# Performance work log

Hardware: AMD Instinct MI355X
Metric: run time of the kernel (lower is better)

Reference implementation:

```python
import jax, jax.numpy as jnp
import numpy as np

B, S, H, NH = 16, 2048, 256, 4
HD = H // NH  # head_size = 64
NEG = -(2.0 ** 32) + 1.0


def _heads(x):
    # [B,S,H] -> [NH,B,S,HD], matching torch.cat(torch.split(x, HD, dim=2), dim=0)
    b, s, _ = x.shape
    return jnp.transpose(x.reshape(b, s, NH, HD), (2, 0, 1, 3))


def setup_inputs() -> dict:
    key = jax.random.key(0)
    ks = jax.random.split(key, 9)
    d = {
        "queries": jax.random.normal(ks[0], (B, S, H), jnp.float32),
        "keys": jax.random.normal(ks[1], (B, S, H), jnp.float32),
        "neighbor_matrix": jax.random.normal(ks[2], (B, S, H), jnp.float32),
        "neighAt_matrix": jax.random.normal(ks[3], (B, S, H), jnp.float32),
        "abs_pos_K": jax.random.normal(ks[4], (B, S, H), jnp.float32),
        "abs_pos_V": jax.random.normal(ks[5], (B, S, H), jnp.float32),
        # True = masked; causal mask (mask strictly-upper triangle)
        "attn_mask": jnp.triu(jnp.ones((S, S), bool), k=1),
        "Qw": jax.random.normal(ks[6], (H, H), jnp.float32) * (1.0 / np.sqrt(H)),
        "Qb": jnp.zeros((H,), jnp.float32),
        "Kw": jax.random.normal(ks[7], (H, H), jnp.float32) * (1.0 / np.sqrt(H)),
        "Kb": jnp.zeros((H,), jnp.float32),
        "Vw": jax.random.normal(ks[8], (H, H), jnp.float32) * (1.0 / np.sqrt(H)),
        "Vb": jnp.zeros((H,), jnp.float32),
    }
    return d


def reference(queries, keys, neighbor_matrix, neighAt_matrix, abs_pos_K, abs_pos_V,
              attn_mask, Qw, Qb, Kw, Kb, Vw, Vb):
    Q = queries @ Qw.T + Qb
    K = keys @ Kw.T + Kb
    V = keys @ Vw.T + Vb

    Qh = _heads(Q)                 # [NH,B,S,HD]
    Kh = _heads(K)
    Vh = _heads(V)
    Nh = _heads(neighbor_matrix)
    Ah = _heads(neighAt_matrix)
    PKh = _heads(abs_pos_K)
    PVh = _heads(abs_pos_V)

    # sum of four QX^T terms == Q @ (K+N+A+PK)^T  (distributivity)
    Ksum = Kh + Nh + Ah + PKh
    scores = jnp.einsum("hbqd,hbkd->hbqk", Qh, Ksum) / jnp.sqrt(jnp.float32(HD))
    scores = jnp.where(attn_mask[None, None], jnp.float32(NEG), scores)
    attn = jax.nn.softmax(scores, axis=-1)

    Vsum = Vh + Nh + Ah + PVh
    out = jnp.einsum("hbqk,hbkd->hbqd", attn, Vsum)   # [NH,B,S,HD]
    # recombine heads along feature dim
    return jnp.transpose(out, (1, 2, 0, 3)).reshape(B, S, H)
```

## Files before the change

### kernel.cpp

```cpp
#include <hip/hip_runtime.h>
#include <math.h>

#define BB 16
#define SS 2048
#define HH 256
#define NHEAD 4
#define HDIM 64

typedef _Float16 f16;
typedef _Float16 f16x2 __attribute__((ext_vector_type(2)));
typedef _Float16 f16x4 __attribute__((ext_vector_type(4)));
typedef _Float16 f16x8 __attribute__((ext_vector_type(8)));
typedef float f32x4 __attribute__((ext_vector_type(4)));

#define MFMA16(a, b, c) __builtin_amdgcn_mfma_f32_16x16x32_f16((a), (b), (c), 0, 0, 0)

__device__ __forceinline__ void split8(const float* p, f16x8& h, f16x8& lo) {
    float4 v0 = *(const float4*)p;
    float4 v1 = *(const float4*)(p + 4);
    float vv[8] = {v0.x, v0.y, v0.z, v0.w, v1.x, v1.y, v1.z, v1.w};
#pragma unroll
    for (int j = 0; j < 8; j++) {
        f16 hv = (f16)vv[j];
        h[j] = hv;
        lo[j] = (f16)(vv[j] - (float)hv);
    }
}

__global__ __launch_bounds__(512) void proj_kernel(
    const float* __restrict__ queries, const float* __restrict__ keys,
    const float* __restrict__ neighbor, const float* __restrict__ neighAt,
    const float* __restrict__ posK, const float* __restrict__ posV,
    const float* __restrict__ Qw, const float* __restrict__ Qb,
    const float* __restrict__ Kw, const float* __restrict__ Kb,
    const float* __restrict__ Vw, const float* __restrict__ Vb,
    f16* __restrict__ Qh, f16* __restrict__ Ql,
    f16* __restrict__ Kh, f16* __restrict__ Kl,
    f16* __restrict__ VTh, f16* __restrict__ VTl)
{
    const int z  = blockIdx.y;
    const int m0 = blockIdx.x * 128;

    const float* X    = (z == 0) ? queries : keys;
    const float* W    = (z == 0) ? Qw : (z == 1 ? Kw : Vw);
    const float* bias = (z == 0) ? Qb : (z == 1 ? Kb : Vb);

    __shared__ __align__(16) char smraw[61440];
    f16*   Xh_s = (f16*)smraw;
    f16*   Xl_s = Xh_s + 128 * 40;
    f16*   Wh_s = Xl_s + 128 * 40;
    f16*   Wl_s = Wh_s + 256 * 40;
    float* Ls   = (float*)smraw;

    const int t  = threadIdx.x;
    const int w  = t >> 6, l = t & 63, c = l & 15, g = l >> 4;
    const int wm = w >> 2, wn = w & 3;

    f32x4 acc[4][4];
#pragma unroll
    for (int i = 0; i < 4; i++)
#pragma unroll
        for (int j = 0; j < 4; j++) acc[i][j] = (f32x4){0.f, 0.f, 0.f, 0.f};

    const int xrow = t >> 2, xseg = t & 3;
    const int wrow = t >> 1, whalf = t & 1;

    for (int ks = 0; ks < 8; ks++) {
        const int k0 = ks * 32;
        __syncthreads();
        {
            f16x8 h, lo;
            split8(&X[(size_t)(m0 + xrow) * HH + k0 + xseg * 8], h, lo);
            *(f16x8*)&Xh_s[xrow * 40 + xseg * 8] = h;
            *(f16x8*)&Xl_s[xrow * 40 + xseg * 8] = lo;
        }
#pragma unroll
        for (int s2 = 0; s2 < 2; s2++) {
            f16x8 h, lo;
            split8(&W[(size_t)wrow * HH + k0 + whalf * 16 + s2 * 8], h, lo);
            *(f16x8*)&Wh_s[wrow * 40 + whalf * 16 + s2 * 8] = h;
            *(f16x8*)&Wl_s[wrow * 40 + whalf * 16 + s2 * 8] = lo;
        }
        __syncthreads();

        f16x8 ah[4], al[4], bh[4], bl[4];
#pragma unroll
        for (int fm = 0; fm < 4; fm++) {
            const int ro = (wm * 64 + fm * 16 + c) * 40 + g * 8;
            ah[fm] = *(const f16x8*)&Xh_s[ro];
            al[fm] = *(const f16x8*)&Xl_s[ro];
        }
#pragma unroll
        for (int fn = 0; fn < 4; fn++) {
            const int ro = (wn * 64 + fn * 16 + c) * 40 + g * 8;
            bh[fn] = *(const f16x8*)&Wh_s[ro];
            bl[fn] = *(const f16x8*)&Wl_s[ro];
        }
#pragma unroll
        for (int fm = 0; fm < 4; fm++)
#pragma unroll
            for (int fn = 0; fn < 4; fn++) {
                acc[fm][fn] = MFMA16(ah[fm], bh[fn], acc[fm][fn]);
                acc[fm][fn] = MFMA16(al[fm], bh[fn], acc[fm][fn]);
                acc[fm][fn] = MFMA16(ah[fm], bl[fn], acc[fm][fn]);
            }
    }

    const int bI  = m0 >> 11;
    const int s0g = m0 & (SS - 1);

#pragma unroll 1
    for (int p = 0; p < 4; p++) {
        __syncthreads();
        if (wm == (p >> 1)) {
            const int fmb = (p & 1) * 2;
#pragma unroll
            for (int fi = 0; fi < 2; fi++)
#pragma unroll
                for (int fn = 0; fn < 4; fn++)
#pragma unroll
                    for (int r = 0; r < 4; r++)
                        Ls[(fi * 16 + 4 * g + r) * 260 + wn * 64 + fn * 16 + c] =
                            acc[fmb + fi][fn][r];
        }
        __syncthreads();

        if (z <= 1) {
            f16* Xph = (z == 0) ? Qh : Kh;
            f16* Xpl = (z == 0) ? Ql : Kl;
#pragma unroll
            for (int i = 0; i < 4; i++) {
                int idx = t + 512 * i;
                int r = idx >> 6, q = idx & 63;
                float4 v  = *(const float4*)&Ls[r * 260 + q * 4];
                float4 bv = *(const float4*)&bias[q * 4];
                v.x += bv.x; v.y += bv.y; v.z += bv.z; v.w += bv.w;
                size_t gg = (size_t)(m0 + 32 * p + r) * HH + q * 4;
                if (z == 1) {
                    float4 n1 = *(const float4*)&neighbor[gg];
                    float4 n2 = *(const float4*)&neighAt[gg];
                    float4 n3 = *(const float4*)&posK[gg];
                    v.x += n1.x + n2.x + n3.x;  v.y += n1.y + n2.y + n3.y;
                    v.z += n1.z + n2.z + n3.z;  v.w += n1.w + n2.w + n3.w;
                }
                f16x4 hv, lv;
                hv[0] = (f16)v.x; hv[1] = (f16)v.y; hv[2] = (f16)v.z; hv[3] = (f16)v.w;
                lv[0] = (f16)(v.x - (float)hv[0]);
                lv[1] = (f16)(v.y - (float)hv[1]);
                lv[2] = (f16)(v.z - (float)hv[2]);
                lv[3] = (f16)(v.w - (float)hv[3]);
                *(f16x4*)(Xph + gg) = hv;
                *(f16x4*)(Xpl + gg) = lv;
            }
        } else {
#pragma unroll
            for (int i = 0; i < 4; i++) {
                int idx = t + 512 * i;
                int r = idx >> 6, q = idx & 63;
                float4 v  = *(const float4*)&Ls[r * 260 + q * 4];
                float4 bv = *(const float4*)&bias[q * 4];
                size_t gg = (size_t)(m0 + 32 * p + r) * HH + q * 4;
                float4 n1 = *(const float4*)&neighbor[gg];
                float4 n2 = *(const float4*)&neighAt[gg];
                float4 n3 = *(const float4*)&posV[gg];
                v.x += bv.x + n1.x + n2.x + n3.x;
                v.y += bv.y + n1.y + n2.y + n3.y;
                v.z += bv.z + n1.z + n2.z + n3.z;
                v.w += bv.w + n1.w + n2.w + n3.w;
                *(float4*)&Ls[r * 260 + q * 4] = v;
            }
            __syncthreads();
            const int n = t >> 1, soff = (t & 1) * 16;
            f16x8 h0, h1, l0, l1;
#pragma unroll
            for (int j = 0; j < 16; j++) {
                float val = Ls[(soff + j) * 260 + n];
                f16 hv = (f16)val;
                f16 lv = (f16)(val - (float)hv);
                if (j < 8) { h0[j] = hv; l0[j] = lv; }
                else       { h1[j - 8] = hv; l1[j - 8] = lv; }
            }
            size_t ga = ((size_t)n * BB + bI) * SS + s0g + 32 * p + soff;
            *(f16x8*)&VTh[ga]     = h0;
            *(f16x8*)&VTh[ga + 8] = h1;
            *(f16x8*)&VTl[ga]     = l0;
            *(f16x8*)&VTl[ga + 8] = l1;
        }
    }
}

__global__ __launch_bounds__(512) void attn_kernel(
    const f16* __restrict__ Qhg, const f16* __restrict__ Qlg,
    const f16* __restrict__ Khg, const f16* __restrict__ Klg,
    const f16* __restrict__ Vhg, const f16* __restrict__ Vlg,
    float* __restrict__ outp)
{
    const int bid = blockIdx.x;
    const int qt  = 15 - (bid >> 6);
    const int rem = bid & 63;
    const int b   = rem >> 2;
    const int h   = rem & 3;
    const int q0  = qt * 128;

    __shared__ __align__(16) f16 smh[46080];
    f16* Qh_s = smh;
    f16* Ql_s = smh + 9216;
    f16* Kh_s = smh + 18432;
    f16* Kl_s = smh + 23040;
    f16* Vh_s = smh + 27648;
    f16* Vl_s = smh + 32256;
    f16* Ps   = smh + 36864;

    const int t = threadIdx.x;

    {
        const size_t base = ((size_t)(b * SS) + q0) * HH + h * 64;
#pragma unroll
        for (int p = 0; p < 2; p++) {
            int idx = t + 512 * p;
            int row = idx >> 3, ch = idx & 7;
            size_t g = base + (size_t)row * HH + ch * 8;
            *(uint4*)&Qh_s[row * 72 + ch * 8] = *(const uint4*)&Qhg[g];
            *(uint4*)&Ql_s[row * 72 + ch * 8] = *(const uint4*)&Qlg[g];
        }
    }
    __syncthreads();

    const int w = t >> 6, l = t & 63, c = l & 15, g = l >> 4;

    f16x8 aQh[2], aQl[2];
#pragma unroll
    for (int dk = 0; dk < 2; dk++) {
        aQh[dk] = *(const f16x8*)&Qh_s[(16 * w + c) * 72 + dk * 32 + g * 8];
        aQl[dk] = *(const f16x8*)&Ql_s[(16 * w + c) * 72 + dk * 32 + g * 8];
    }

    f32x4 o[4] = {{0.f,0.f,0.f,0.f},{0.f,0.f,0.f,0.f},{0.f,0.f,0.f,0.f},{0.f,0.f,0.f,0.f}};
    float m_i[4] = {-INFINITY, -INFINITY, -INFINITY, -INFINITY};
    float l_i[4] = {0.f, 0.f, 0.f, 0.f};

    const int nkv = 2 * qt + 2;
    for (int kt = 0; kt < nkv; kt++) {
        const int k0 = kt * 64;
        __syncthreads();
        {
            int row = t >> 3, ch = t & 7;
            size_t gk = ((size_t)(b * SS) + k0 + row) * HH + h * 64 + ch * 8;
            *(uint4*)&Kh_s[row * 72 + ch * 8] = *(const uint4*)&Khg[gk];
            *(uint4*)&Kl_s[row * 72 + ch * 8] = *(const uint4*)&Klg[gk];
            size_t gv = ((size_t)(h * 64 + row) * BB + b) * SS + k0 + ch * 8;
            *(uint4*)&Vh_s[row * 72 + ch * 8] = *(const uint4*)&Vhg[gv];
            *(uint4*)&Vl_s[row * 72 + ch * 8] = *(const uint4*)&Vlg[gv];
        }
        __syncthreads();

        if (q0 + 16 * w + 15 < k0) continue;

        f32x4 sacc[4] = {{0.f,0.f,0.f,0.f},{0.f,0.f,0.f,0.f},{0.f,0.f,0.f,0.f},{0.f,0.f,0.f,0.f}};
#pragma unroll
        for (int cb = 0; cb < 4; cb++) {
#pragma unroll
            for (int dk = 0; dk < 2; dk++) {
                const int ro = (16 * cb + c) * 72 + dk * 32 + g * 8;
                f16x8 bh = *(const f16x8*)&Kh_s[ro];
                f16x8 bl = *(const f16x8*)&Kl_s[ro];
                sacc[cb] = MFMA16(aQh[dk], bh, sacc[cb]);
                sacc[cb] = MFMA16(aQl[dk], bh, sacc[cb]);
                sacc[cb] = MFMA16(aQh[dk], bl, sacc[cb]);
            }
        }

        const bool needMask = (k0 + 63) > (q0 + 16 * w);
#pragma unroll
        for (int r = 0; r < 4; r++) {
            const int q = q0 + 16 * w + 4 * g + r;
            float s[4];
            float mloc = -INFINITY;
#pragma unroll
            for (int cb = 0; cb < 4; cb++) {
                float sv = sacc[cb][r] * 0.125f;
                if (needMask && (k0 + 16 * cb + c > q)) sv = -INFINITY;
                s[cb] = sv;
                mloc = fmaxf(mloc, sv);
            }
            mloc = fmaxf(mloc, __shfl_xor(mloc, 1, 16));
            mloc = fmaxf(mloc, __shfl_xor(mloc, 2, 16));
            mloc = fmaxf(mloc, __shfl_xor(mloc, 4, 16));
            mloc = fmaxf(mloc, __shfl_xor(mloc, 8, 16));
            float mn = fmaxf(m_i[r], mloc);
            float al = __expf(m_i[r] - mn);
            float pv[4];
            float psum = 0.f;
#pragma unroll
            for (int cb = 0; cb < 4; cb++) {
                pv[cb] = __expf(s[cb] - mn);
                psum += pv[cb];
            }
            psum += __shfl_xor(psum, 1, 16);
            psum += __shfl_xor(psum, 2, 16);
            psum += __shfl_xor(psum, 4, 16);
            psum += __shfl_xor(psum, 8, 16);
            l_i[r] = l_i[r] * al + psum;
            m_i[r] = mn;
#pragma unroll
            for (int cb = 0; cb < 4; cb++) o[cb][r] *= al;

            const int prow = (16 * w + 4 * g + r) * 72;
#pragma unroll
            for (int cb = 0; cb < 4; cb++) {
                float pn = __shfl_xor(pv[cb], 1);
                if (!(c & 1)) {
                    f16x2 pk;
                    pk[0] = (f16)pv[cb];
                    pk[1] = (f16)pn;
                    *(f16x2*)&Ps[prow + 16 * cb + c] = pk;
                }
            }
        }

        f16x8 aP[2];
#pragma unroll
        for (int kk = 0; kk < 2; kk++)
            aP[kk] = *(const f16x8*)&Ps[(16 * w + c) * 72 + kk * 32 + g * 8];
#pragma unroll
        for (int cb = 0; cb < 4; cb++) {
#pragma unroll
            for (int kk = 0; kk < 2; kk++) {
                const int ro = (16 * cb + c) * 72 + kk * 32 + g * 8;
                f16x8 bh = *(const f16x8*)&Vh_s[ro];
                f16x8 bl = *(const f16x8*)&Vl_s[ro];
                o[cb] = MFMA16(aP[kk], bh, o[cb]);
                o[cb] = MFMA16(aP[kk], bl, o[cb]);
            }
        }
    }

#pragma unroll
    for (int r = 0; r < 4; r++) {
        float inv = 1.0f / l_i[r];
        size_t rowb = ((size_t)(b * SS) + q0 + 16 * w + 4 * g + r) * HH + h * 64;
#pragma unroll
        for (int cb = 0; cb < 4; cb++)
            outp[rowb + 16 * cb + c] = o[cb][r] * inv;
    }
}

extern "C" void kernel_launch(void* const* d_in, const int* in_sizes, int n_in,
                              void* d_out, int out_size, void* d_ws, size_t ws_size,
                              hipStream_t stream) {
    const float* queries  = (const float*)d_in[0];
    const float* keys     = (const float*)d_in[1];
    const float* neighbor = (const float*)d_in[2];
    const float* neighAt  = (const float*)d_in[3];
    const float* posK     = (const float*)d_in[4];
    const float* posV     = (const float*)d_in[5];
    const float* Qw = (const float*)d_in[7];
    const float* Qb = (const float*)d_in[8];
    const float* Kw = (const float*)d_in[9];
    const float* Kb = (const float*)d_in[10];
    const float* Vw = (const float*)d_in[11];
    const float* Vb = (const float*)d_in[12];

    const size_t NEL = (size_t)BB * SS * HH;
    f16* wsh = (f16*)d_ws;
    f16* Qh  = wsh;
    f16* Ql  = wsh + NEL;
    f16* Kh  = wsh + 2 * NEL;
    f16* Kl  = wsh + 3 * NEL;
    f16* VTh = wsh + 4 * NEL;
    f16* VTl = wsh + 5 * NEL;

    dim3 g1((BB * SS) / 128, 3, 1);
    proj_kernel<<<g1, dim3(512), 0, stream>>>(queries, keys, neighbor, neighAt,
                                              posK, posV, Qw, Qb, Kw, Kb, Vw, Vb,
                                              Qh, Ql, Kh, Kl, VTh, VTl);

    dim3 g2(16 * BB * NHEAD, 1, 1);
    attn_kernel<<<g2, dim3(512), 0, stream>>>(Qh, Ql, Kh, Kl, VTh, VTl,
                                              (float*)d_out);
}
```

Baseline: 657.6 us.

## Pre-split weights once, shrink attention tiles, and prefetch K/V into registers

A small kernel now converts Qw/Kw/Vw to high/low f16 pairs once, using the output buffer as scratch, so the projection kernel loads f16 weights instead of re-splitting fp32 weights in every block. The attention kernel moves from 128-query, 512-thread blocks to 64-query, 256-thread blocks with a launch-bounds occupancy hint. Q fragments load straight from global memory into registers, and the next K/V tile is fetched into registers while the current tile is computed, then written to LDS. This aims to hide global-load latency, balance causal work better and cut conversion work, at the cost of more registers and twice as many K/V tile reloads across blocks.

```diff
diff --git a/kernel.cpp b/kernel.cpp
--- a/kernel.cpp
+++ b/kernel.cpp
@@ -27,13 +27,26 @@
     }
 }
 
+__global__ __launch_bounds__(256) void splitw_kernel(
+    const float* __restrict__ Qw, const float* __restrict__ Kw,
+    const float* __restrict__ Vw, f16* __restrict__ Wh, f16* __restrict__ Wl)
+{
+    int i = blockIdx.x * 256 + threadIdx.x;
+    const float* src = (i < 8192) ? Qw : (i < 16384 ? Kw : Vw);
+    int off = (i & 8191) * 8;
+    f16x8 h, lo;
+    split8(&src[off], h, lo);
+    *(f16x8*)&Wh[(size_t)i * 8] = h;
+    *(f16x8*)&Wl[(size_t)i * 8] = lo;
+}
+
 __global__ __launch_bounds__(512) void proj_kernel(
     const float* __restrict__ queries, const float* __restrict__ keys,
     const float* __restrict__ neighbor, const float* __restrict__ neighAt,
     const float* __restrict__ posK, const float* __restrict__ posV,
-    const float* __restrict__ Qw, const float* __restrict__ Qb,
-    const float* __restrict__ Kw, const float* __restrict__ Kb,
-    const float* __restrict__ Vw, const float* __restrict__ Vb,
+    const f16* __restrict__ Whp, const f16* __restrict__ Wlp,
+    const float* __restrict__ Qb, const float* __restrict__ Kb,
+    const float* __restrict__ Vb,
     f16* __restrict__ Qh, f16* __restrict__ Ql,
     f16* __restrict__ Kh, f16* __restrict__ Kl,
     f16* __restrict__ VTh, f16* __restrict__ VTl)
@@ -42,8 +55,9 @@
     const int m0 = blockIdx.x * 128;
 
     const float* X    = (z == 0) ? queries : keys;
-    const float* W    = (z == 0) ? Qw : (z == 1 ? Kw : Vw);
     const float* bias = (z == 0) ? Qb : (z == 1 ? Kb : Vb);
+    const f16*   Whz  = Whp + (size_t)z * 65536;
+    const f16*   Wlz  = Wlp + (size_t)z * 65536;
 
     __shared__ __align__(16) char smraw[61440];
     f16*   Xh_s = (f16*)smraw;
@@ -63,7 +77,6 @@
         for (int j = 0; j < 4; j++) acc[i][j] = (f32x4){0.f, 0.f, 0.f, 0.f};
 
     const int xrow = t >> 2, xseg = t & 3;
-    const int wrow = t >> 1, whalf = t & 1;
 
     for (int ks = 0; ks < 8; ks++) {
         const int k0 = ks * 32;
@@ -75,11 +88,13 @@
             *(f16x8*)&Xl_s[xrow * 40 + xseg * 8] = lo;
         }
 #pragma unroll
-        for (int s2 = 0; s2 < 2; s2++) {
-            f16x8 h, lo;
-            split8(&W[(size_t)wrow * HH + k0 + whalf * 16 + s2 * 8], h, lo);
-            *(f16x8*)&Wh_s[wrow * 40 + whalf * 16 + s2 * 8] = h;
-            *(f16x8*)&Wl_s[wrow * 40 + whalf * 16 + s2 * 8] = lo;
+        for (int p = 0; p < 2; p++) {
+            int idx = t + 512 * p;
+            int row = idx >> 2, seg = idx & 3;
+            *(f16x8*)&Wh_s[row * 40 + seg * 8] =
+                *(const f16x8*)&Whz[(size_t)row * HH + k0 + seg * 8];
+            *(f16x8*)&Wl_s[row * 40 + seg * 8] =
+                *(const f16x8*)&Wlz[(size_t)row * HH + k0 + seg * 8];
         }
         __syncthreads();
 
@@ -189,72 +204,78 @@
     }
 }
 
-__global__ __launch_bounds__(512) void attn_kernel(
+__global__ __launch_bounds__(256, 3) void attn_kernel(
     const f16* __restrict__ Qhg, const f16* __restrict__ Qlg,
     const f16* __restrict__ Khg, const f16* __restrict__ Klg,
     const f16* __restrict__ Vhg, const f16* __restrict__ Vlg,
     float* __restrict__ outp)
 {
     const int bid = blockIdx.x;
-    const int qt  = 15 - (bid >> 6);
+    const int qt  = 31 - (bid >> 6);
     const int rem = bid & 63;
     const int b   = rem >> 2;
     const int h   = rem & 3;
-    const int q0  = qt * 128;
-
-    __shared__ __align__(16) f16 smh[46080];
-    f16* Qh_s = smh;
-    f16* Ql_s = smh + 9216;
-    f16* Kh_s = smh + 18432;
-    f16* Kl_s = smh + 23040;
-    f16* Vh_s = smh + 27648;
-    f16* Vl_s = smh + 32256;
-    f16* Ps   = smh + 36864;
+    const int q0  = qt * 64;
+
+    __shared__ __align__(16) f16 smh[23040];
+    f16* Kh_s = smh;
+    f16* Kl_s = smh + 4608;
+    f16* Vh_s = smh + 9216;
+    f16* Vl_s = smh + 13824;
+    f16* Ps   = smh + 18432;
 
     const int t = threadIdx.x;
-
+    const int w = t >> 6, l = t & 63, c = l & 15, g = l >> 4;
+
+    f16x8 aQh[2], aQl[2];
     {
-        const size_t base = ((size_t)(b * SS) + q0) * HH + h * 64;
-#pragma unroll
-        for (int p = 0; p < 2; p++) {
-            int idx = t + 512 * p;
-            int row = idx >> 3, ch = idx & 7;
-            size_t g = base + (size_t)row * HH + ch * 8;
-            *(uint4*)&Qh_s[row * 72 + ch * 8] = *(const uint4*)&Qhg[g];
-            *(uint4*)&Ql_s[row * 72 + ch * 8] = *(const uint4*)&Qlg[g];
-        }
-    }
+        const size_t qrow = ((size_t)(b * SS) + q0 + 16 * w + c) * HH + h * 64;
+        aQh[0] = *(const f16x8*)&Qhg[qrow + g * 8];
+        aQh[1] = *(const f16x8*)&Qhg[qrow + 32 + g * 8];
+        aQl[0] = *(const f16x8*)&Qlg[qrow + g * 8];
+        aQl[1] = *(const f16x8*)&Qlg[qrow + 32 + g * 8];
+    }
+
+    const int srow = t >> 3, sch = t & 7;
+
+    uint4 kr[8];
+#define ISSUE_LOADS(k0v)                                                      \
+    {                                                                         \
+        _Pragma("unroll")                                                     \
+        for (int p = 0; p < 2; p++) {                                         \
+            const int row = srow + 32 * p;                                    \
+            size_t gk = ((size_t)(b * SS) + (k0v) + row) * HH + h * 64 + sch * 8; \
+            size_t gv = (((size_t)h * 64 + row) * BB + b) * SS + (k0v) + sch * 8; \
+            kr[4 * p + 0] = *(const uint4*)&Khg[gk];                          \
+            kr[4 * p + 1] = *(const uint4*)&Klg[gk];                          \
+            kr[4 * p + 2] = *(const uint4*)&Vhg[gv];                          \
+            kr[4 * p + 3] = *(const uint4*)&Vlg[gv];                          \
+        }                                                                     \
+    }
+#define WRITE_LDS()                                                           \
+    {                                                                         \
+        _Pragma("unroll")                                                     \
+        for (int p = 0; p < 2; p++) {                                         \
+            const int ro = (srow + 32 * p) * 72 + sch * 8;                    \
+            *(uint4*)&Kh_s[ro] = kr[4 * p + 0];                               \
+            *(uint4*)&Kl_s[ro] = kr[4 * p + 1];                               \
+            *(uint4*)&Vh_s[ro] = kr[4 * p + 2];                               \
+            *(uint4*)&Vl_s[ro] = kr[4 * p + 3];                               \
+        }                                                                     \
+    }
+
+    ISSUE_LOADS(0);
+    WRITE_LDS();
     __syncthreads();
-
-    const int w = t >> 6, l = t & 63, c = l & 15, g = l >> 4;
-
-    f16x8 aQh[2], aQl[2];
-#pragma unroll
-    for (int dk = 0; dk < 2; dk++) {
-        aQh[dk] = *(const f16x8*)&Qh_s[(16 * w + c) * 72 + dk * 32 + g * 8];
-        aQl[dk] = *(const f16x8*)&Ql_s[(16 * w + c) * 72 + dk * 32 + g * 8];
-    }
 
     f32x4 o[4] = {{0.f,0.f,0.f,0.f},{0.f,0.f,0.f,0.f},{0.f,0.f,0.f,0.f},{0.f,0.f,0.f,0.f}};
     float m_i[4] = {-INFINITY, -INFINITY, -INFINITY, -INFINITY};
     float l_i[4] = {0.f, 0.f, 0.f, 0.f};
 
-    const int nkv = 2 * qt + 2;
+    const int nkv = qt + 1;
     for (int kt = 0; kt < nkv; kt++) {
         const int k0 = kt * 64;
-        __syncthreads();
-        {
-            int row = t >> 3, ch = t & 7;
-            size_t gk = ((size_t)(b * SS) + k0 + row) * HH + h * 64 + ch * 8;
-            *(uint4*)&Kh_s[row * 72 + ch * 8] = *(const uint4*)&Khg[gk];
-            *(uint4*)&Kl_s[row * 72 + ch * 8] = *(const uint4*)&Klg[gk];
-            size_t gv = ((size_t)(h * 64 + row) * BB + b) * SS + k0 + ch * 8;
-            *(uint4*)&Vh_s[row * 72 + ch * 8] = *(const uint4*)&Vhg[gv];
-            *(uint4*)&Vl_s[row * 72 + ch * 8] = *(const uint4*)&Vlg[gv];
-        }
-        __syncthreads();
-
-        if (q0 + 16 * w + 15 < k0) continue;
+        if (kt + 1 < nkv) ISSUE_LOADS(k0 + 64);
 
         f32x4 sacc[4] = {{0.f,0.f,0.f,0.f},{0.f,0.f,0.f,0.f},{0.f,0.f,0.f,0.f},{0.f,0.f,0.f,0.f}};
 #pragma unroll
@@ -270,7 +291,7 @@
             }
         }
 
-        const bool needMask = (k0 + 63) > (q0 + 16 * w);
+        const bool needMask = (kt == qt);
 #pragma unroll
         for (int r = 0; r < 4; r++) {
             const int q = q0 + 16 * w + 4 * g + r;
@@ -333,6 +354,12 @@
                 o[cb] = MFMA16(aP[kk], bl, o[cb]);
             }
         }
+
+        if (kt + 1 < nkv) {
+            __syncthreads();
+            WRITE_LDS();
+            __syncthreads();
+        }
     }
 
 #pragma unroll
@@ -343,6 +370,8 @@
         for (int cb = 0; cb < 4; cb++)
             outp[rowb + 16 * cb + c] = o[cb][r] * inv;
     }
+#undef ISSUE_LOADS
+#undef WRITE_LDS
 }
 
 extern "C" void kernel_launch(void* const* d_in, const int* in_sizes, int n_in,
@@ -369,13 +398,17 @@
     f16* Kl  = wsh + 3 * NEL;
     f16* VTh = wsh + 4 * NEL;
     f16* VTl = wsh + 5 * NEL;
+    f16* Wh  = (f16*)d_out;
+    f16* Wl  = Wh + 3 * 65536;
+
+    splitw_kernel<<<dim3(96), dim3(256), 0, stream>>>(Qw, Kw, Vw, Wh, Wl);
 
     dim3 g1((BB * SS) / 128, 3, 1);
     proj_kernel<<<g1, dim3(512), 0, stream>>>(queries, keys, neighbor, neighAt,
-                                              posK, posV, Qw, Qb, Kw, Kb, Vw, Vb,
+                                              posK, posV, Wh, Wl, Qb, Kb, Vb,
                                               Qh, Ql, Kh, Kl, VTh, VTl);
 
-    dim3 g2(16 * BB * NHEAD, 1, 1);
-    attn_kernel<<<g2, dim3(512), 0, stream>>>(Qh, Ql, Kh, Kl, VTh, VTl,
+    dim3 g2(32 * BB * NHEAD, 1, 1);
+    attn_kernel<<<g2, dim3(256), 0, stream>>>(Qh, Ql, Kh, Kl, VTh, VTl,
                                               (float*)d_out);
 }
```

After: 797.9 us. 1.21x slower.
